# Kernel optimization log

Measured on AMD Instinct MI355X. Metric: run time of the kernel, lower is better.

## Reference

```python
import jax, jax.numpy as jnp
import numpy as np

TOPK = 2  # config.topk_exp


def setup_inputs() -> dict:
    key = jax.random.key(0)
    ks = jax.random.split(key, 4)
    B, S, D, F, E = 4, 1024, 768, 3072, 8
    scale_in = 1.0 / np.sqrt(D)
    scale_hid = 1.0 / np.sqrt(F)
    return {
        "x": jax.random.normal(ks[0], (B, S, D), dtype=jnp.float32),
        "router_w": jax.random.normal(ks[1], (E, D), dtype=jnp.float32) * scale_in,
        "w_fc": jax.random.normal(ks[2], (E, D, F), dtype=jnp.float32) * scale_in,
        "b_fc": jnp.zeros((E, F), dtype=jnp.float32),
        "w_proj": jax.random.normal(ks[3], (E, F, D), dtype=jnp.float32) * scale_hid,
        "b_proj": jnp.zeros((E, D), dtype=jnp.float32),
    }


def _moe_forward(x, router_w, w_fc, b_fc, w_proj, b_proj):
    B, S, D = x.shape
    E = router_w.shape[0]
    xt = x.reshape(-1, D)  # [T, D] tokens
    # per-token router: Linear(D, E, bias=False)
    gate_logits = xt @ router_w.T  # [T, E]
    # topk_exp > 1: raw logits -> topk -> softmax over the k selected logits
    weights, selected = jax.lax.top_k(gate_logits, TOPK)  # [T, k]
    weights = jax.nn.softmax(weights.astype(jnp.float32), axis=1).astype(x.dtype)
    # combine weights per expert: w[t, e] = sum_k weights[t,k] * (selected[t,k]==e)
    onehot = jax.nn.one_hot(selected, E, dtype=x.dtype)  # [T, k, E]
    comb = jnp.einsum('tk,tke->te', weights, onehot)  # [T, E]
    # expert MLP (GPT-2 style: fc -> gelu -> proj), evaluated densely then combined
    h = jax.nn.gelu(jnp.einsum('td,edf->etf', xt, w_fc) + b_fc[:, None, :], approximate=False)
    y = jnp.einsum('etf,efd->etd', h, w_proj) + b_proj[:, None, :]  # [E, T, D]
    out = jnp.einsum('te,etd->td', comb, y)  # weighted scatter-combine
    return out.reshape(B, S, D)


def reference(x, router_w, w_fc, b_fc, w_proj, b_proj):
    return _moe_forward(x, router_w, w_fc, b_fc, w_proj, b_proj)
```

## Files before the change

### kernel.cpp

```cpp
#include <hip/hip_runtime.h>
#include <hip/hip_bf16.h>

#define TT 4096
#define DD 768
#define FF 3072
#define EE 8
#define NSLOT 8192
#define NSLOT_PAD 8320

typedef __attribute__((ext_vector_type(8))) short bf16x8;
typedef __attribute__((ext_vector_type(4))) float f32x4;
typedef const __attribute__((address_space(1))) void* gas1_t;
typedef __attribute__((address_space(3))) void* las3_t;

__global__ __launch_bounds__(256) void router2_kernel(const float* __restrict__ x,
    const float* __restrict__ rw, int* __restrict__ tokE, float* __restrict__ tokW,
    int* __restrict__ blkCnt) {
  __shared__ float rws[EE * 832];
  __shared__ int cnt_s[EE];
  int tid = threadIdx.x;
  if (tid < EE) cnt_s[tid] = 0;
#pragma unroll
  for (int k = 0; k < 6; ++k) {
    int c = tid + k * 256;
    int e = c / 192, rem = c % 192;
    int s = rem / 12, i = rem % 12;
    float4 v = *(const float4*)&rw[e * DD + s * 48 + i * 4];
    *(float4*)&rws[e * 832 + s * 52 + i * 4] = v;
  }
  __syncthreads();
  int lane = tid & 63;
  int sl = lane & 15;
  int t = blockIdx.x * 16 + (tid >> 6) * 4 + (lane >> 4);
  const float4* xp = (const float4*)(x + (size_t)t * DD + sl * 48);
  float acc[EE];
#pragma unroll
  for (int e = 0; e < EE; ++e) acc[e] = 0.f;
#pragma unroll
  for (int i = 0; i < 12; ++i) {
    float4 xv = xp[i];
#pragma unroll
    for (int e = 0; e < EE; ++e) {
      float4 rv = *(const float4*)&rws[e * 832 + sl * 52 + i * 4];
      acc[e] = fmaf(xv.x, rv.x, fmaf(xv.y, rv.y, fmaf(xv.z, rv.z, fmaf(xv.w, rv.w, acc[e]))));
    }
  }
#pragma unroll
  for (int off = 8; off > 0; off >>= 1) {
#pragma unroll
    for (int e = 0; e < EE; ++e) acc[e] += __shfl_xor(acc[e], off);
  }
  if (sl == 0) {
    float v0 = -1e30f; int e0 = 0;
#pragma unroll
    for (int e = 0; e < EE; ++e) { if (acc[e] > v0) { v0 = acc[e]; e0 = e; } }
    float v1 = -1e30f; int e1 = 0;
#pragma unroll
    for (int e = 0; e < EE; ++e) { if (e != e0 && acc[e] > v1) { v1 = acc[e]; e1 = e; } }
    float w1 = 1.f / (1.f + __expf(v0 - v1));
    float w0 = 1.f - w1;
    tokE[2 * t] = e0; tokE[2 * t + 1] = e1;
    tokW[2 * t] = w0; tokW[2 * t + 1] = w1;
    atomicAdd(&cnt_s[e0], 1);
    atomicAdd(&cnt_s[e1], 1);
  }
  __syncthreads();
  if (tid < EE) blkCnt[blockIdx.x * EE + tid] = cnt_s[tid];
}

__global__ __launch_bounds__(256) void offsets2_kernel(const int* __restrict__ blkCnt,
    int* __restrict__ offs, int* __restrict__ blkBase,
    int* __restrict__ tile1, int* __restrict__ tile2, int* __restrict__ meta) {
  __shared__ int wsum[4][EE];
  int tid = threadIdx.x;
  int lane = tid & 63, w = tid >> 6;
  int c[EE], s[EE];
#pragma unroll
  for (int e = 0; e < EE; ++e) { c[e] = blkCnt[tid * EE + e]; s[e] = c[e]; }
#pragma unroll
  for (int off = 1; off < 64; off <<= 1) {
#pragma unroll
    for (int e = 0; e < EE; ++e) {
      int v = __shfl_up(s[e], off);
      if (lane >= off) s[e] += v;
    }
  }
  if (lane == 63) {
#pragma unroll
    for (int e = 0; e < EE; ++e) wsum[w][e] = s[e];
  }
  __syncthreads();
#pragma unroll
  for (int e = 0; e < EE; ++e) {
    int pre = 0;
    for (int w2 = 0; w2 < w; ++w2) pre += wsum[w2][e];
    s[e] += pre;
  }
  int tot[EE];
#pragma unroll
  for (int e = 0; e < EE; ++e) tot[e] = wsum[0][e] + wsum[1][e] + wsum[2][e] + wsum[3][e];
  int offl[EE + 1];
  offl[0] = 0;
#pragma unroll
  for (int e = 0; e < EE; ++e) offl[e + 1] = offl[e] + tot[e];
#pragma unroll
  for (int e = 0; e < EE; ++e) blkBase[tid * EE + e] = offl[e] + s[e] - c[e];
  if (tid == 0) {
    for (int e = 0; e <= EE; ++e) offs[e] = offl[e];
    int n1 = 0, n2 = 0;
    for (int e = 0; e < EE; ++e) { n1 += (tot[e] + 127) / 128; n2 += (tot[e] + 63) / 64; }
    meta[0] = n1; meta[1] = n2;
  }
  if (tid < EE) {
    int p1 = 0, p2 = 0;
    for (int e = 0; e < tid; ++e) { p1 += (tot[e] + 127) / 128; p2 += (tot[e] + 63) / 64; }
    for (int m = 0; m < tot[tid]; m += 128) tile1[p1++] = (tid << 20) | m;
    for (int m = 0; m < tot[tid]; m += 64)  tile2[p2++] = (tid << 20) | m;
  }
}

__global__ __launch_bounds__(256) void scatter_gather2_kernel(const float* __restrict__ x,
    const int* __restrict__ tokE, const float* __restrict__ tokW,
    const int* __restrict__ blkBase, int* __restrict__ slotIdx, float* __restrict__ slotW,
    __hip_bfloat16* __restrict__ Xg) {
  __shared__ int base_s[EE], lcur[EE];
  __shared__ int sl_s[16][2];
  int tid = threadIdx.x;
  int b = blockIdx.x;
  if (tid < EE) { base_s[tid] = blkBase[b * EE + tid]; lcur[tid] = 0; }
  __syncthreads();
  if (tid < 16) {
    int t = b * 16 + tid;
    int e0 = tokE[2 * t], e1 = tokE[2 * t + 1];
    int s0 = base_s[e0] + atomicAdd(&lcur[e0], 1);
    int s1 = base_s[e1] + atomicAdd(&lcur[e1], 1);
    slotIdx[2 * t] = s0; slotIdx[2 * t + 1] = s1;
    slotW[s0] = tokW[2 * t]; slotW[s1] = tokW[2 * t + 1];
    sl_s[tid][0] = s0; sl_s[tid][1] = s1;
  }
  __syncthreads();
  int k = tid >> 4, p = tid & 15;
  int t = b * 16 + k;
  int s0 = sl_s[k][0], s1 = sl_s[k][1];
  const float4* src = (const float4*)(x + (size_t)t * DD + p * 48);
  ushort4* d0 = (ushort4*)(Xg + (size_t)s0 * DD + p * 48);
  ushort4* d1 = (ushort4*)(Xg + (size_t)s1 * DD + p * 48);
#pragma unroll
  for (int i = 0; i < 12; ++i) {
    float4 v = src[i];
    union { ushort4 u; __hip_bfloat16 h[4]; } cv;
    cv.h[0] = __float2bfloat16(v.x);
    cv.h[1] = __float2bfloat16(v.y);
    cv.h[2] = __float2bfloat16(v.z);
    cv.h[3] = __float2bfloat16(v.w);
    d0[i] = cv.u;
    d1[i] = cv.u;
  }
}

__global__ void transpose_convert_kernel(const float* __restrict__ w_fc, __hip_bfloat16* __restrict__ wfcT,
                                         const float* __restrict__ w_proj, __hip_bfloat16* __restrict__ wprojT) {
  __shared__ float tile[64][65];
  int bx = blockIdx.x;
  const float* S; __hip_bfloat16* D; int K, N, n0, k0;
  if (bx < 576) { S = w_fc;   D = wfcT;   K = DD; N = FF; n0 = (bx % 48) * 64; k0 = (bx / 48) * 64; }
  else { bx -= 576; S = w_proj; D = wprojT; K = FF; N = DD; n0 = (bx % 12) * 64; k0 = (bx / 12) * 64; }
  S += (size_t)blockIdx.z * K * N;
  D += (size_t)blockIdx.z * K * N;
  int tid = threadIdx.x;
#pragma unroll
  for (int i = 0; i < 4; ++i) {
    int slot = i * 256 + tid;
    int r = slot >> 4, c4 = slot & 15;
    float4 v = *(const float4*)&S[(size_t)(k0 + r) * N + n0 + c4 * 4];
    tile[r][c4 * 4 + 0] = v.x; tile[r][c4 * 4 + 1] = v.y;
    tile[r][c4 * 4 + 2] = v.z; tile[r][c4 * 4 + 3] = v.w;
  }
  __syncthreads();
#pragma unroll
  for (int i = 0; i < 4; ++i) {
    int slot = i * 256 + tid;
    int n = slot >> 4, kc = slot & 15;
    union { ushort4 u; __hip_bfloat16 h[4]; } cv;
    cv.h[0] = __float2bfloat16(tile[kc * 4 + 0][n]);
    cv.h[1] = __float2bfloat16(tile[kc * 4 + 1][n]);
    cv.h[2] = __float2bfloat16(tile[kc * 4 + 2][n]);
    cv.h[3] = __float2bfloat16(tile[kc * 4 + 3][n]);
    *(ushort4*)&D[(size_t)(n0 + n) * K + k0 + kc * 4] = cv.u;
  }
}

template <int ROWS>
__device__ __forceinline__ void stage_tile(const short* gsrc, int ldk, short* lds, int tid) {
#pragma unroll
  for (int it = 0; it < ROWS / 32; ++it) {
    int fs = tid + it * 256;
    int m = fs >> 3;
    int c = (fs & 7) ^ (m & 7);
    __builtin_amdgcn_global_load_lds((gas1_t)(gsrc + (size_t)m * ldk + c * 8),
                                     (las3_t)(lds + fs * 8), 16, 0, 0);
  }
}

__device__ __forceinline__ float gelu_f(float v) {
  float z = v * 0.70710678118654752f;
  float az = fabsf(z);
  float t = 1.0f / (1.0f + 0.3275911f * az);
  float poly = t * (0.254829592f + t * (-0.284496736f + t * (1.421413741f +
               t * (-1.453152027f + t * 1.061405429f))));
  float erf_abs = 1.0f - poly * __expf(-az * az);
  float erf = copysignf(erf_abs, z);
  return 0.5f * v * (1.0f + erf);
}

__global__ __launch_bounds__(256) void gemm1_kernel(const __hip_bfloat16* __restrict__ Xg,
    const __hip_bfloat16* __restrict__ wfcT, const float* __restrict__ b_fc,
    __hip_bfloat16* __restrict__ H, const int* __restrict__ offs,
    const int* __restrict__ tile1, const int* __restrict__ meta) {
  __shared__ __align__(16) short As[128 * 64];
  __shared__ __align__(16) short Bs[128 * 64];
  if ((int)blockIdx.y >= meta[0]) return;
  int tv = tile1[blockIdx.y];
  int e = tv >> 20;
  int m_base = tv & 0xFFFFF;
  int off_e = offs[e];
  int n_e = offs[e + 1] - off_e;
  int n0 = blockIdx.x * 128;
  const short* A = (const short*)Xg + (size_t)(off_e + m_base) * DD;
  const short* B = (const short*)wfcT + (size_t)e * FF * DD + (size_t)n0 * DD;
  int tid = threadIdx.x;
  int lane = tid & 63, wid = tid >> 6;
  int l15 = lane & 15, q = lane >> 4;
  int wm = wid & 1, wn = wid >> 1;
  f32x4 acc[4][4] = {};
  for (int kk = 0; kk < DD; kk += 64) {
    stage_tile<128>(A + kk, DD, As, tid);
    stage_tile<128>(B + kk, DD, Bs, tid);
    __builtin_amdgcn_s_waitcnt(0);
    __syncthreads();
#pragma unroll
    for (int ks = 0; ks < 2; ++ks) {
      bf16x8 af[4], bfr[4];
#pragma unroll
      for (int mi = 0; mi < 4; ++mi) {
        int m = wm * 64 + mi * 16 + l15;
        int s = ((ks << 2) + q) ^ (m & 7);
        af[mi] = *(const bf16x8*)&As[m * 64 + s * 8];
      }
#pragma unroll
      for (int ni = 0; ni < 4; ++ni) {
        int n = wn * 64 + ni * 16 + l15;
        int s = ((ks << 2) + q) ^ (n & 7);
        bfr[ni] = *(const bf16x8*)&Bs[n * 64 + s * 8];
      }
#pragma unroll
      for (int mi = 0; mi < 4; ++mi)
#pragma unroll
        for (int ni = 0; ni < 4; ++ni)
          acc[mi][ni] = __builtin_amdgcn_mfma_f32_16x16x32_bf16(af[mi], bfr[ni], acc[mi][ni], 0, 0, 0);
    }
    __syncthreads();
  }
  __hip_bfloat16* Hp = H + (size_t)(off_e + m_base) * FF + n0;
#pragma unroll
  for (int mi = 0; mi < 4; ++mi) {
#pragma unroll
    for (int r = 0; r < 4; ++r) {
      int ml = wm * 64 + mi * 16 + q * 4 + r;
      if (m_base + ml < n_e) {
#pragma unroll
        for (int ni = 0; ni < 4; ++ni) {
          int nl = wn * 64 + ni * 16 + l15;
          float v = acc[mi][ni][r] + b_fc[e * FF + n0 + nl];
          Hp[(size_t)ml * FF + nl] = __float2bfloat16(gelu_f(v));
        }
      }
    }
  }
}

__global__ __launch_bounds__(256) void gemm2_kernel(const __hip_bfloat16* __restrict__ H,
    const __hip_bfloat16* __restrict__ wprojT, const float* __restrict__ b_proj,
    const float* __restrict__ slotW, float* __restrict__ Yw, const int* __restrict__ offs,
    const int* __restrict__ tile2, const int* __restrict__ meta) {
  __shared__ __align__(16) short As[64 * 64];
  __shared__ __align__(16) short Bs[128 * 64];
  if ((int)blockIdx.y >= meta[1]) return;
  int tv = tile2[blockIdx.y];
  int e = tv >> 20;
  int m_base = tv & 0xFFFFF;
  int off_e = offs[e];
  int n_e = offs[e + 1] - off_e;
  int n0 = blockIdx.x * 128;
  const short* A = (const short*)H + (size_t)(off_e + m_base) * FF;
  const short* B = (const short*)wprojT + (size_t)e * DD * FF + (size_t)n0 * FF;
  int tid = threadIdx.x;
  int lane = tid & 63, wid = tid >> 6;
  int l15 = lane & 15, q = lane >> 4;
  int wm = wid & 1, wn = wid >> 1;
  f32x4 acc[2][4] = {};
  for (int kk = 0; kk < FF; kk += 64) {
    stage_tile<64>(A + kk, FF, As, tid);
    stage_tile<128>(B + kk, FF, Bs, tid);
    __builtin_amdgcn_s_waitcnt(0);
    __syncthreads();
#pragma unroll
    for (int ks = 0; ks < 2; ++ks) {
      bf16x8 af[2], bfr[4];
#pragma unroll
      for (int mi = 0; mi < 2; ++mi) {
        int m = wm * 32 + mi * 16 + l15;
        int s = ((ks << 2) + q) ^ (m & 7);
        af[mi] = *(const bf16x8*)&As[m * 64 + s * 8];
      }
#pragma unroll
      for (int ni = 0; ni < 4; ++ni) {
        int n = wn * 64 + ni * 16 + l15;
        int s = ((ks << 2) + q) ^ (n & 7);
        bfr[ni] = *(const bf16x8*)&Bs[n * 64 + s * 8];
      }
#pragma unroll
      for (int mi = 0; mi < 2; ++mi)
#pragma unroll
        for (int ni = 0; ni < 4; ++ni)
          acc[mi][ni] = __builtin_amdgcn_mfma_f32_16x16x32_bf16(af[mi], bfr[ni], acc[mi][ni], 0, 0, 0);
    }
    __syncthreads();
  }
  float* Yp = Yw + (size_t)(off_e + m_base) * DD + n0;
#pragma unroll
  for (int mi = 0; mi < 2; ++mi) {
#pragma unroll
    for (int r = 0; r < 4; ++r) {
      int ml = wm * 32 + mi * 16 + q * 4 + r;
      if (m_base + ml < n_e) {
        float w = slotW[off_e + m_base + ml];
#pragma unroll
        for (int ni = 0; ni < 4; ++ni) {
          int nl = wn * 64 + ni * 16 + l15;
          Yp[(size_t)ml * DD + nl] = w * (acc[mi][ni][r] + b_proj[e * DD + n0 + nl]);
        }
      }
    }
  }
}

__global__ void combine_kernel(const float* __restrict__ Yw, const int* __restrict__ slotIdx,
                               float* __restrict__ out) {
  int idx = blockIdx.x * 256 + threadIdx.x;
  int t = idx / (DD / 4);
  int g = idx - t * (DD / 4);
  int s0 = slotIdx[2 * t], s1 = slotIdx[2 * t + 1];
  const float4 a = ((const float4*)(Yw + (size_t)s0 * DD))[g];
  const float4 b = ((const float4*)(Yw + (size_t)s1 * DD))[g];
  float4 o;
  o.x = a.x + b.x; o.y = a.y + b.y; o.z = a.z + b.z; o.w = a.w + b.w;
  ((float4*)(out + (size_t)t * DD))[g] = o;
}

extern "C" void kernel_launch(void* const* d_in, const int* in_sizes, int n_in,
                              void* d_out, int out_size, void* d_ws, size_t ws_size,
                              hipStream_t stream) {
  const float* x        = (const float*)d_in[0];
  const float* router_w = (const float*)d_in[1];
  const float* w_fc     = (const float*)d_in[2];
  const float* b_fc     = (const float*)d_in[3];
  const float* w_proj   = (const float*)d_in[4];
  const float* b_proj   = (const float*)d_in[5];
  float* out = (float*)d_out;

  char* p = (char*)d_ws;
  auto alloc = [&](size_t bytes) {
    char* r = p;
    p += (bytes + 255) & ~(size_t)255;
    return r;
  };
  __hip_bfloat16* wfcT   = (__hip_bfloat16*)alloc((size_t)EE * FF * DD * 2);
  __hip_bfloat16* wprojT = (__hip_bfloat16*)alloc((size_t)EE * DD * FF * 2);
  __hip_bfloat16* Xg     = (__hip_bfloat16*)alloc((size_t)NSLOT_PAD * DD * 2);
  __hip_bfloat16* H      = (__hip_bfloat16*)alloc((size_t)NSLOT_PAD * FF * 2);
  float*          Yw     = (float*)alloc((size_t)NSLOT_PAD * DD * 4);
  int*   tokE    = (int*)alloc(TT * 2 * 4);
  float* tokW    = (float*)alloc(TT * 2 * 4);
  int*   slotIdx = (int*)alloc(TT * 2 * 4);
  float* slotW   = (float*)alloc(NSLOT_PAD * 4);
  int*   blkCnt  = (int*)alloc(256 * EE * 4);
  int*   blkBase = (int*)alloc(256 * EE * 4);
  int*   tile1   = (int*)alloc(128 * 4);
  int*   tile2   = (int*)alloc(256 * 4);
  int*   offs    = (int*)alloc(64);
  int*   meta    = (int*)alloc(64);

  router2_kernel<<<256, 256, 0, stream>>>(x, router_w, tokE, tokW, blkCnt);
  offsets2_kernel<<<1, 256, 0, stream>>>(blkCnt, offs, blkBase, tile1, tile2, meta);
  scatter_gather2_kernel<<<256, 256, 0, stream>>>(x, tokE, tokW, blkBase, slotIdx, slotW, Xg);
  transpose_convert_kernel<<<dim3(1152, 1, EE), 256, 0, stream>>>(w_fc, wfcT, w_proj, wprojT);
  gemm1_kernel<<<dim3(FF / 128, 72), 256, 0, stream>>>(Xg, wfcT, b_fc, H, offs, tile1, meta);
  gemm2_kernel<<<dim3(DD / 128, 136), 256, 0, stream>>>(H, wprojT, b_proj, slotW, Yw, offs, tile2, meta);
  combine_kernel<<<TT * (DD / 4) / 256, 256, 0, stream>>>(Yw, slotIdx, out);
}
```

Baseline: 395.2 us.

## Double-buffer LDS tiles with BK=32 and async prefetch in both expert GEMMs

Both grouped GEMM kernels switch from a single 64-wide K tile with a full waitcnt(0) and two barriers per step to a double-buffered 32-wide K tile. The next tile is prefetched with global_load_lds while the current one feeds MFMA, using a partial vmcnt wait and a 4-chunk swizzle. Global and LDS addresses are precomputed outside the loop, and bias loads are hoisted out of the epilogue. The aim is to hide global memory latency behind compute, at the cost of twice as many loop iterations and barriers per K, and reliance on hand-encoded waitcnt immediates.

Measured after the change: 397.3 us. No clear change (+0.5%).

```diff
diff --git a/kernel.cpp b/kernel.cpp
--- a/kernel.cpp
+++ b/kernel.cpp
@@ -7,6 +7,9 @@
 #define EE 8
 #define NSLOT 8192
 #define NSLOT_PAD 8320
+
+#define WAITCNT_VM4 0x0F74
+#define WAITCNT_VM3 0x0F73
 
 typedef __attribute__((ext_vector_type(8))) short bf16x8;
 typedef __attribute__((ext_vector_type(4))) float f32x4;
@@ -190,18 +193,6 @@
   }
 }
 
-template <int ROWS>
-__device__ __forceinline__ void stage_tile(const short* gsrc, int ldk, short* lds, int tid) {
-#pragma unroll
-  for (int it = 0; it < ROWS / 32; ++it) {
-    int fs = tid + it * 256;
-    int m = fs >> 3;
-    int c = (fs & 7) ^ (m & 7);
-    __builtin_amdgcn_global_load_lds((gas1_t)(gsrc + (size_t)m * ldk + c * 8),
-                                     (las3_t)(lds + fs * 8), 16, 0, 0);
-  }
-}
-
 __device__ __forceinline__ float gelu_f(float v) {
   float z = v * 0.70710678118654752f;
   float az = fabsf(z);
@@ -213,12 +204,14 @@
   return 0.5f * v * (1.0f + erf);
 }
 
+__device__ __forceinline__ int swz4(int m) { return (m + (m >> 2)) & 3; }
+
 __global__ __launch_bounds__(256) void gemm1_kernel(const __hip_bfloat16* __restrict__ Xg,
     const __hip_bfloat16* __restrict__ wfcT, const float* __restrict__ b_fc,
     __hip_bfloat16* __restrict__ H, const int* __restrict__ offs,
     const int* __restrict__ tile1, const int* __restrict__ meta) {
-  __shared__ __align__(16) short As[128 * 64];
-  __shared__ __align__(16) short Bs[128 * 64];
+  __shared__ __align__(16) short As[2][128 * 32];
+  __shared__ __align__(16) short Bs[2][128 * 32];
   if ((int)blockIdx.y >= meta[0]) return;
   int tv = tile1[blockIdx.y];
   int e = tv >> 20;
@@ -232,35 +225,56 @@
   int lane = tid & 63, wid = tid >> 6;
   int l15 = lane & 15, q = lane >> 4;
   int wm = wid & 1, wn = wid >> 1;
+  int fs0 = tid, fs1 = tid + 256;
+  int m0 = fs0 >> 2, c0 = (fs0 & 3) ^ swz4(m0);
+  int m1 = fs1 >> 2, c1 = (fs1 & 3) ^ swz4(m1);
+  const short* gA0 = A + (size_t)m0 * DD + c0 * 8;
+  const short* gA1 = A + (size_t)m1 * DD + c1 * 8;
+  const short* gB0 = B + (size_t)m0 * DD + c0 * 8;
+  const short* gB1 = B + (size_t)m1 * DD + c1 * 8;
+  int aoff[4], boff[4];
+#pragma unroll
+  for (int mi = 0; mi < 4; ++mi) {
+    int r = wm * 64 + mi * 16 + l15;
+    aoff[mi] = (r * 4 + (q ^ swz4(r))) * 8;
+  }
+#pragma unroll
+  for (int ni = 0; ni < 4; ++ni) {
+    int r = wn * 64 + ni * 16 + l15;
+    boff[ni] = (r * 4 + (q ^ swz4(r))) * 8;
+  }
   f32x4 acc[4][4] = {};
-  for (int kk = 0; kk < DD; kk += 64) {
-    stage_tile<128>(A + kk, DD, As, tid);
-    stage_tile<128>(B + kk, DD, Bs, tid);
-    __builtin_amdgcn_s_waitcnt(0);
-    __syncthreads();
-#pragma unroll
-    for (int ks = 0; ks < 2; ++ks) {
-      bf16x8 af[4], bfr[4];
-#pragma unroll
-      for (int mi = 0; mi < 4; ++mi) {
-        int m = wm * 64 + mi * 16 + l15;
-        int s = ((ks << 2) + q) ^ (m & 7);
-        af[mi] = *(const bf16x8*)&As[m * 64 + s * 8];
-      }
-#pragma unroll
-      for (int ni = 0; ni < 4; ++ni) {
-        int n = wn * 64 + ni * 16 + l15;
-        int s = ((ks << 2) + q) ^ (n & 7);
-        bfr[ni] = *(const bf16x8*)&Bs[n * 64 + s * 8];
-      }
-#pragma unroll
-      for (int mi = 0; mi < 4; ++mi)
-#pragma unroll
-        for (int ni = 0; ni < 4; ++ni)
-          acc[mi][ni] = __builtin_amdgcn_mfma_f32_16x16x32_bf16(af[mi], bfr[ni], acc[mi][ni], 0, 0, 0);
-    }
-    __syncthreads();
-  }
+  __builtin_amdgcn_global_load_lds((gas1_t)gA0, (las3_t)(&As[0][0] + fs0 * 8), 16, 0, 0);
+  __builtin_amdgcn_global_load_lds((gas1_t)gA1, (las3_t)(&As[0][0] + fs1 * 8), 16, 0, 0);
+  __builtin_amdgcn_global_load_lds((gas1_t)gB0, (las3_t)(&Bs[0][0] + fs0 * 8), 16, 0, 0);
+  __builtin_amdgcn_global_load_lds((gas1_t)gB1, (las3_t)(&Bs[0][0] + fs1 * 8), 16, 0, 0);
+  gA0 += 32; gA1 += 32; gB0 += 32; gB1 += 32;
+  for (int it = 0; it < DD / 32; ++it) {
+    int cur = it & 1, nxt = cur ^ 1;
+    short* curA = &As[cur][0];
+    short* curB = &Bs[cur][0];
+    __builtin_amdgcn_s_barrier();
+    __builtin_amdgcn_global_load_lds((gas1_t)gA0, (las3_t)(&As[nxt][0] + fs0 * 8), 16, 0, 0);
+    __builtin_amdgcn_global_load_lds((gas1_t)gA1, (las3_t)(&As[nxt][0] + fs1 * 8), 16, 0, 0);
+    __builtin_amdgcn_global_load_lds((gas1_t)gB0, (las3_t)(&Bs[nxt][0] + fs0 * 8), 16, 0, 0);
+    __builtin_amdgcn_global_load_lds((gas1_t)gB1, (las3_t)(&Bs[nxt][0] + fs1 * 8), 16, 0, 0);
+    gA0 += 32; gA1 += 32; gB0 += 32; gB1 += 32;
+    __builtin_amdgcn_s_waitcnt(WAITCNT_VM4);
+    __builtin_amdgcn_s_barrier();
+    bf16x8 af[4], bfr[4];
+#pragma unroll
+    for (int mi = 0; mi < 4; ++mi) af[mi] = *(const bf16x8*)(curA + aoff[mi]);
+#pragma unroll
+    for (int ni = 0; ni < 4; ++ni) bfr[ni] = *(const bf16x8*)(curB + boff[ni]);
+#pragma unroll
+    for (int mi = 0; mi < 4; ++mi)
+#pragma unroll
+      for (int ni = 0; ni < 4; ++ni)
+        acc[mi][ni] = __builtin_amdgcn_mfma_f32_16x16x32_bf16(af[mi], bfr[ni], acc[mi][ni], 0, 0, 0);
+  }
+  float bias[4];
+#pragma unroll
+  for (int ni = 0; ni < 4; ++ni) bias[ni] = b_fc[e * FF + n0 + wn * 64 + ni * 16 + l15];
   __hip_bfloat16* Hp = H + (size_t)(off_e + m_base) * FF + n0;
 #pragma unroll
   for (int mi = 0; mi < 4; ++mi) {
@@ -271,7 +285,7 @@
 #pragma unroll
         for (int ni = 0; ni < 4; ++ni) {
           int nl = wn * 64 + ni * 16 + l15;
-          float v = acc[mi][ni][r] + b_fc[e * FF + n0 + nl];
+          float v = acc[mi][ni][r] + bias[ni];
           Hp[(size_t)ml * FF + nl] = __float2bfloat16(gelu_f(v));
         }
       }
@@ -283,8 +297,8 @@
     const __hip_bfloat16* __restrict__ wprojT, const float* __restrict__ b_proj,
     const float* __restrict__ slotW, float* __restrict__ Yw, const int* __restrict__ offs,
     const int* __restrict__ tile2, const int* __restrict__ meta) {
-  __shared__ __align__(16) short As[64 * 64];
-  __shared__ __align__(16) short Bs[128 * 64];
+  __shared__ __align__(16) short As[2][64 * 32];
+  __shared__ __align__(16) short Bs[2][128 * 32];
   if ((int)blockIdx.y >= meta[1]) return;
   int tv = tile2[blockIdx.y];
   int e = tv >> 20;
@@ -298,35 +312,53 @@
   int lane = tid & 63, wid = tid >> 6;
   int l15 = lane & 15, q = lane >> 4;
   int wm = wid & 1, wn = wid >> 1;
+  int fs0 = tid, fs1 = tid + 256;
+  int m0 = fs0 >> 2, c0 = (fs0 & 3) ^ swz4(m0);
+  int m1 = fs1 >> 2, c1 = (fs1 & 3) ^ swz4(m1);
+  const short* gA0 = A + (size_t)m0 * FF + c0 * 8;
+  const short* gB0 = B + (size_t)m0 * FF + c0 * 8;
+  const short* gB1 = B + (size_t)m1 * FF + c1 * 8;
+  int aoff[2], boff[4];
+#pragma unroll
+  for (int mi = 0; mi < 2; ++mi) {
+    int r = wm * 32 + mi * 16 + l15;
+    aoff[mi] = (r * 4 + (q ^ swz4(r))) * 8;
+  }
+#pragma unroll
+  for (int ni = 0; ni < 4; ++ni) {
+    int r = wn * 64 + ni * 16 + l15;
+    boff[ni] = (r * 4 + (q ^ swz4(r))) * 8;
+  }
   f32x4 acc[2][4] = {};
-  for (int kk = 0; kk < FF; kk += 64) {
-    stage_tile<64>(A + kk, FF, As, tid);
-    stage_tile<128>(B + kk, FF, Bs, tid);
-    __builtin_amdgcn_s_waitcnt(0);
-    __syncthreads();
-#pragma unroll
-    for (int ks = 0; ks < 2; ++ks) {
-      bf16x8 af[2], bfr[4];
-#pragma unroll
-      for (int mi = 0; mi < 2; ++mi) {
-        int m = wm * 32 + mi * 16 + l15;
-        int s = ((ks << 2) + q) ^ (m & 7);
-        af[mi] = *(const bf16x8*)&As[m * 64 + s * 8];
-      }
-#pragma unroll
-      for (int ni = 0; ni < 4; ++ni) {
-        int n = wn * 64 + ni * 16 + l15;
-        int s = ((ks << 2) + q) ^ (n & 7);
-        bfr[ni] = *(const bf16x8*)&Bs[n * 64 + s * 8];
-      }
-#pragma unroll
-      for (int mi = 0; mi < 2; ++mi)
-#pragma unroll
-        for (int ni = 0; ni < 4; ++ni)
-          acc[mi][ni] = __builtin_amdgcn_mfma_f32_16x16x32_bf16(af[mi], bfr[ni], acc[mi][ni], 0, 0, 0);
-    }
-    __syncthreads();
-  }
+  __builtin_amdgcn_global_load_lds((gas1_t)gA0, (las3_t)(&As[0][0] + fs0 * 8), 16, 0, 0);
+  __builtin_amdgcn_global_load_lds((gas1_t)gB0, (las3_t)(&Bs[0][0] + fs0 * 8), 16, 0, 0);
+  __builtin_amdgcn_global_load_lds((gas1_t)gB1, (las3_t)(&Bs[0][0] + fs1 * 8), 16, 0, 0);
+  gA0 += 32; gB0 += 32; gB1 += 32;
+  for (int it = 0; it < FF / 32; ++it) {
+    int cur = it & 1, nxt = cur ^ 1;
+    short* curA = &As[cur][0];
+    short* curB = &Bs[cur][0];
+    __builtin_amdgcn_s_barrier();
+    __builtin_amdgcn_global_load_lds((gas1_t)gA0, (las3_t)(&As[nxt][0] + fs0 * 8), 16, 0, 0);
+    __builtin_amdgcn_global_load_lds((gas1_t)gB0, (las3_t)(&Bs[nxt][0] + fs0 * 8), 16, 0, 0);
+    __builtin_amdgcn_global_load_lds((gas1_t)gB1, (las3_t)(&Bs[nxt][0] + fs1 * 8), 16, 0, 0);
+    gA0 += 32; gB0 += 32; gB1 += 32;
+    __builtin_amdgcn_s_waitcnt(WAITCNT_VM3);
+    __builtin_amdgcn_s_barrier();
+    bf16x8 af[2], bfr[4];
+#pragma unroll
+    for (int mi = 0; mi < 2; ++mi) af[mi] = *(const bf16x8*)(curA + aoff[mi]);
+#pragma unroll
+    for (int ni = 0; ni < 4; ++ni) bfr[ni] = *(const bf16x8*)(curB + boff[ni]);
+#pragma unroll
+    for (int mi = 0; mi < 2; ++mi)
+#pragma unroll
+      for (int ni = 0; ni < 4; ++ni)
+        acc[mi][ni] = __builtin_amdgcn_mfma_f32_16x16x32_bf16(af[mi], bfr[ni], acc[mi][ni], 0, 0, 0);
+  }
+  float bias[4];
+#pragma unroll
+  for (int ni = 0; ni < 4; ++ni) bias[ni] = b_proj[e * DD + n0 + wn * 64 + ni * 16 + l15];
   float* Yp = Yw + (size_t)(off_e + m_base) * DD + n0;
 #pragma unroll
   for (int mi = 0; mi < 2; ++mi) {
@@ -338,7 +370,7 @@
 #pragma unroll
         for (int ni = 0; ni < 4; ++ni) {
           int nl = wn * 64 + ni * 16 + l15;
-          Yp[(size_t)ml * DD + nl] = w * (acc[mi][ni][r] + b_proj[e * DD + n0 + nl]);
+          Yp[(size_t)ml * DD + nl] = w * (acc[mi][ni][r] + bias[ni]);
         }
       }
     }
```
